# Kernel tuning notes

Hardware: AMD Instinct MI355X
Metric: run time of the kernel (lower is better)

## Reference

```python
import jax, jax.numpy as jnp
import numpy as np


def setup_inputs() -> dict:
    key = jax.random.key(0)
    k1, k2, k3 = jax.random.split(key, 3)
    N1, N2, P, D = 4, 8, 1024, 128  # P = PH*PW = 32*32 (512px / 16 patch)
    feats = jax.random.normal(k1, (N1, P, D), dtype=jnp.float32)
    nfeats = jax.random.normal(k2, (N2, P, D), dtype=jnp.float32)
    background_masks = jax.random.uniform(k3, (N1, P), dtype=jnp.float32)
    return {"feats": feats, "nfeats": nfeats, "background_masks": background_masks,
            "PH": 32, "PW": 32, "H": 512, "W": 512}


def reference(feats, nfeats, background_masks, PH, PW, H, W):
    # L2-normalize patch embeddings (as in `f / f.norm(dim=-1, keepdim=True)`)
    f = feats / jnp.linalg.norm(feats, axis=-1, keepdims=True)    # [N1,P,D]
    g = nfeats / jnp.linalg.norm(nfeats, axis=-1, keepdims=True)  # [N2,Q,D]
    # Euclidean cdist of unit vectors: d^2 = 2 - 2*dot (clamped at 0)
    dot = jnp.einsum('npd,mqd->nmpq', f, g)                        # [N1,N2,P,Q]
    dist = jnp.sqrt(jnp.maximum(2.0 - 2.0 * dot, 0.0)) / 2.0      # cdist/2, permuted
    # min over normal patches Q -> per-query-patch nearest-neighbor distance
    scores_patch = dist.min(axis=-1)                               # [N1,N2,P]
    scores_patch = scores_patch * background_masks[:, None, :]
    # image score: max over query patches, mean over normal images
    scores = scores_patch.max(axis=-1).mean(axis=-1)               # [N1]
    # pixel map: mean over normal images, reshape to patch grid, bilinear upsample
    sp = scores_patch.mean(axis=1).reshape(-1, PH, PW)             # [N1,PH,PW]
    scores_pixel = jax.image.resize(sp, (sp.shape[0], H, W), method='bilinear')
    return scores, scores_pixel
```

## Files before the change

### kernel.cpp

```cpp
#include <hip/hip_runtime.h>

typedef __attribute__((ext_vector_type(8))) short short8;
typedef __attribute__((ext_vector_type(4))) float f32x4;

typedef const __attribute__((address_space(1))) unsigned int glb_u32;
typedef __attribute__((address_space(3))) unsigned int lds_u32;

static __device__ inline unsigned short f2bf(float x) {
    unsigned int u = __float_as_uint(x);
    u = (u + 0x7FFFu + ((u >> 16) & 1u)) >> 16;
    return (unsigned short)u;
}

__global__ __launch_bounds__(256) void knorm(const float* __restrict__ feats,
                                             const float* __restrict__ nfeats,
                                             unsigned short* __restrict__ fb,
                                             unsigned short* __restrict__ gb) {
    int row = blockIdx.x * 4 + (threadIdx.x >> 6);
    int lane = threadIdx.x & 63;
    const float* src;
    unsigned short* dst;
    if (row < 4096) { src = feats + row * 128;           dst = fb + row * 128; }
    else            { src = nfeats + (row - 4096) * 128; dst = gb + (row - 4096) * 128; }
    float2 v = ((const float2*)src)[lane];
    float ss = v.x * v.x + v.y * v.y;
    #pragma unroll
    for (int d = 32; d; d >>= 1) ss += __shfl_xor(ss, d);
    float inv = 1.0f / sqrtf(ss);
    ushort2 o;
    o.x = f2bf(v.x * inv);
    o.y = f2bf(v.y * inv);
    ((ushort2*)dst)[lane] = o;
}

__global__ __launch_bounds__(512, 2) void kscore(const unsigned short* __restrict__ fb,
                                                 const unsigned short* __restrict__ gb,
                                                 float* __restrict__ sp_part) {
    __shared__ unsigned short gtile[2][32 * 128];
    const int tid = threadIdx.x;
    const int lane = tid & 63;
    const int wave = tid >> 6;
    const int wp = wave >> 1, wqt = wave & 1;
    const int l15 = lane & 15, lhi = lane >> 4;
    const int m = blockIdx.x;
    const int ptile = blockIdx.y >> 1, qh = blockIdx.y & 1;
    const int rowbase = ptile * 256 + wp * 64;

    const unsigned short* gBase = gb + ((size_t)m * 1024 + qh * 512) * 128;

    auto stage = [&](int buf, int qb) {
        int r = tid >> 4, s = tid & 15;
        int scol = s ^ (r & 7);
        __builtin_amdgcn_global_load_lds(
            (glb_u32*)(gBase + (size_t)(qb + r) * 128 + scol * 8),
            (lds_u32*)((char*)gtile[buf] + tid * 16), 16, 0, 0);
    };

    stage(0, 0);
    stage(1, 32);

    short8 a[4][4];
    #pragma unroll
    for (int pg = 0; pg < 4; pg++) {
        const unsigned short* arow = fb + (size_t)(rowbase + pg * 16 + l15) * 128;
        #pragma unroll
        for (int kk = 0; kk < 4; kk++)
            a[pg][kk] = *(const short8*)(arow + kk * 32 + lhi * 8);
    }

    f32x4 mx[4];
    #pragma unroll
    for (int pg = 0; pg < 4; pg++)
        #pragma unroll
        for (int i = 0; i < 4; i++) mx[pg][i] = -1e30f;

    #pragma unroll
    for (int t = 0; t < 16; t++) {
        if (t < 15) asm volatile("s_waitcnt vmcnt(1)" ::: "memory");
        else        asm volatile("s_waitcnt vmcnt(0)" ::: "memory");
        __builtin_amdgcn_s_barrier();
        __builtin_amdgcn_sched_barrier(0);
        const char* tp = (const char*)gtile[t & 1];
        const int r = wqt * 16 + l15;
        const int rowoff = r * 256;
        const int swz = (r & 7) << 4;
        f32x4 acc[4];
        #pragma unroll
        for (int pg = 0; pg < 4; pg++)
            #pragma unroll
            for (int i = 0; i < 4; i++) acc[pg][i] = 0.f;
        #pragma unroll
        for (int kk = 0; kk < 4; kk++) {
            short8 b = *(const short8*)(tp + ((rowoff + kk * 64 + lhi * 16) ^ swz));
            #pragma unroll
            for (int pg = 0; pg < 4; pg++)
                acc[pg] = __builtin_amdgcn_mfma_f32_16x16x32_bf16(a[pg][kk], b, acc[pg], 0, 0, 0);
        }
        #pragma unroll
        for (int pg = 0; pg < 4; pg++)
            #pragma unroll
            for (int i = 0; i < 4; i++) mx[pg][i] = fmaxf(mx[pg][i], acc[pg][i]);
        asm volatile("" ::: "memory");
        __builtin_amdgcn_s_barrier();
        if (t < 14) stage(t & 1, (t + 2) * 32);
    }

    #pragma unroll
    for (int pg = 0; pg < 4; pg++)
        #pragma unroll
        for (int i = 0; i < 4; i++) {
            float v = mx[pg][i];
            v = fmaxf(v, __shfl_xor(v, 1));
            v = fmaxf(v, __shfl_xor(v, 2));
            v = fmaxf(v, __shfl_xor(v, 4));
            v = fmaxf(v, __shfl_xor(v, 8));
            mx[pg][i] = v;
        }
    if (l15 == 0) {
        const int slot = qh * 2 + wqt;
        #pragma unroll
        for (int pg = 0; pg < 4; pg++)
            #pragma unroll
            for (int i = 0; i < 4; i++) {
                int row = rowbase + pg * 16 + lhi * 4 + i;
                int n = row >> 10, p = row & 1023;
                sp_part[((size_t)(n * 8 + m) * 4 + slot) * 1024 + p] = mx[pg][i];
            }
    }
}

__global__ __launch_bounds__(256) void kfinal(const float* __restrict__ sp_part,
                                              const float* __restrict__ mask,
                                              float* __restrict__ out) {
    const int n = blockIdx.y;
    const int bx = blockIdx.x;
    const int t = threadIdx.x;
    float* pix = out + 4;

    if (bx == 64) {
        __shared__ float smax[4];
        float acc = 0.f;
        for (int m = 0; m < 8; m++) {
            const float* base = sp_part + (size_t)(n * 8 + m) * 4 * 1024;
            float lm = -1e30f;
            #pragma unroll
            for (int i = 0; i < 4; i++) {
                int p = i * 256 + t;
                float dot = fmaxf(fmaxf(base[p], base[1024 + p]),
                                  fmaxf(base[2048 + p], base[3072 + p]));
                float d = sqrtf(fmaxf(2.0f - 2.0f * dot, 0.0f)) * 0.5f * mask[n * 1024 + p];
                lm = fmaxf(lm, d);
            }
            #pragma unroll
            for (int d = 32; d; d >>= 1) lm = fmaxf(lm, __shfl_xor(lm, d));
            if ((t & 63) == 0) smax[t >> 6] = lm;
            __syncthreads();
            if (t == 0) acc += fmaxf(fmaxf(smax[0], smax[1]), fmaxf(smax[2], smax[3]));
            __syncthreads();
        }
        if (t == 0) out[n] = acc * 0.125f;
        return;
    }

    __shared__ float sp_row[2][32];
    const int band = bx * 8;
    const int pr_lo = (int)floorf((band + 0.5f) * 0.0625f - 0.5f);
    const int row0 = min(max(pr_lo, 0), 31);
    const int row1 = min(max(pr_lo + 1, 0), 31);
    {
        int v = t >> 2, sub = t & 3;
        int vr = v >> 5, vc = v & 31;
        int p = (vr ? row1 : row0) * 32 + vc;
        float sum = 0.f;
        #pragma unroll
        for (int mi = 0; mi < 2; mi++) {
            int m = sub * 2 + mi;
            const float* base = sp_part + (size_t)(n * 8 + m) * 4 * 1024 + p;
            float dot = fmaxf(fmaxf(base[0], base[1024]),
                              fmaxf(base[2048], base[3072]));
            sum += sqrtf(fmaxf(2.0f - 2.0f * dot, 0.0f)) * 0.5f;
        }
        sum *= mask[n * 1024 + p];
        sum += __shfl_xor(sum, 1);
        sum += __shfl_xor(sum, 2);
        if (sub == 0) sp_row[vr][vc] = sum * 0.125f;
    }
    __syncthreads();
    #pragma unroll
    for (int i = 0; i < 16; i++) {
        int idx = i * 256 + t;
        int yl = idx >> 9, x = idx & 511;
        int y = band + yl;
        float fy = (y + 0.5f) * 0.0625f - 0.5f;
        float ty = fy - (float)pr_lo;
        float fx = (x + 0.5f) * 0.0625f - 0.5f;
        float xf = floorf(fx);
        float tx = fx - xf;
        int x0 = (int)xf;
        int x0c = min(max(x0, 0), 31), x1c = min(max(x0 + 1, 0), 31);
        float v00 = sp_row[0][x0c], v01 = sp_row[0][x1c];
        float v10 = sp_row[1][x0c], v11 = sp_row[1][x1c];
        float v0 = v00 + tx * (v01 - v00);
        float v1 = v10 + tx * (v11 - v10);
        pix[(size_t)n * 262144 + (size_t)y * 512 + x] = v0 + ty * (v1 - v0);
    }
}

extern "C" void kernel_launch(void* const* d_in, const int* in_sizes, int n_in,
                              void* d_out, int out_size, void* d_ws, size_t ws_size,
                              hipStream_t stream) {
    const float* feats = (const float*)d_in[0];
    const float* nfeats = (const float*)d_in[1];
    const float* mask = (const float*)d_in[2];
    float* out = (float*)d_out;

    unsigned short* fb = (unsigned short*)d_ws;
    unsigned short* gb = fb + 4096 * 128;
    float* sp_part = (float*)((char*)d_ws + 3u * 1024u * 1024u);

    knorm<<<3072, 256, 0, stream>>>(feats, nfeats, fb, gb);
    kscore<<<dim3(8, 32), 512, 0, stream>>>(fb, gb, sp_part);
    kfinal<<<dim3(65, 4), 256, 0, stream>>>(sp_part, mask, out);
}
```

Measured before the change: 30.97 us.

## Stage G tiles through registers instead of direct global-to-LDS loads

```diff
diff --git a/kernel.cpp b/kernel.cpp
--- a/kernel.cpp
+++ b/kernel.cpp
@@ -2,9 +2,7 @@
 
 typedef __attribute__((ext_vector_type(8))) short short8;
 typedef __attribute__((ext_vector_type(4))) float f32x4;
-
-typedef const __attribute__((address_space(1))) unsigned int glb_u32;
-typedef __attribute__((address_space(3))) unsigned int lds_u32;
+typedef __attribute__((ext_vector_type(4))) unsigned int u32x4;
 
 static __device__ inline unsigned short f2bf(float x) {
     unsigned int u = __float_as_uint(x);
@@ -36,7 +34,7 @@
 __global__ __launch_bounds__(512, 2) void kscore(const unsigned short* __restrict__ fb,
                                                  const unsigned short* __restrict__ gb,
                                                  float* __restrict__ sp_part) {
-    __shared__ unsigned short gtile[2][32 * 128];
+    __shared__ char gtile[2][8192];
     const int tid = threadIdx.x;
     const int lane = tid & 63;
     const int wave = tid >> 6;
@@ -48,16 +46,9 @@
 
     const unsigned short* gBase = gb + ((size_t)m * 1024 + qh * 512) * 128;
 
-    auto stage = [&](int buf, int qb) {
-        int r = tid >> 4, s = tid & 15;
-        int scol = s ^ (r & 7);
-        __builtin_amdgcn_global_load_lds(
-            (glb_u32*)(gBase + (size_t)(qb + r) * 128 + scol * 8),
-            (lds_u32*)((char*)gtile[buf] + tid * 16), 16, 0, 0);
-    };
-
-    stage(0, 0);
-    stage(1, 32);
+    const int sr = tid >> 4, sc = tid & 15;
+    const unsigned short* gsrc = gBase + (size_t)sr * 128 + sc * 8;
+    const int wofs = (sr * 256 + sc * 16) ^ ((sr & 7) << 4);
 
     short8 a[4][4];
     #pragma unroll
@@ -74,13 +65,19 @@
         #pragma unroll
         for (int i = 0; i < 4; i++) mx[pg][i] = -1e30f;
 
+    u32x4 st0 = *(const u32x4*)(gsrc);
+    *(u32x4*)(gtile[0] + wofs) = st0;
+    u32x4 stn = *(const u32x4*)(gsrc + 32 * 128);
+    asm volatile("s_waitcnt lgkmcnt(0)" ::: "memory");
+    __builtin_amdgcn_s_barrier();
+
     #pragma unroll
     for (int t = 0; t < 16; t++) {
-        if (t < 15) asm volatile("s_waitcnt vmcnt(1)" ::: "memory");
-        else        asm volatile("s_waitcnt vmcnt(0)" ::: "memory");
-        __builtin_amdgcn_s_barrier();
         __builtin_amdgcn_sched_barrier(0);
-        const char* tp = (const char*)gtile[t & 1];
+        u32x4 stnn;
+        if (t < 14) stnn = *(const u32x4*)(gsrc + (size_t)(t + 2) * 32 * 128);
+        if (t < 15) *(u32x4*)(gtile[(t + 1) & 1] + wofs) = stn;
+        const char* tp = gtile[t & 1];
         const int r = wqt * 16 + l15;
         const int rowoff = r * 256;
         const int swz = (r & 7) << 4;
@@ -100,9 +97,9 @@
         for (int pg = 0; pg < 4; pg++)
             #pragma unroll
             for (int i = 0; i < 4; i++) mx[pg][i] = fmaxf(mx[pg][i], acc[pg][i]);
-        asm volatile("" ::: "memory");
+        if (t < 14) stn = stnn;
+        asm volatile("s_waitcnt lgkmcnt(0)" ::: "memory");
         __builtin_amdgcn_s_barrier();
-        if (t < 14) stage(t & 1, (t + 2) * 32);
     }
 
     #pragma unroll
```

New measurement: 31.05 us. No clear change (+0.3%).
